# Kernel optimization log

Hardware: AMD Instinct MI355X
Metric: run time of the kernel (lower is better)

Reference implementation:

```python
import jax, jax.numpy as jnp
import numpy as np

N, E, B, D, H = 5000, 16000, 8, 128, 8
HD = D // H
DD = D // 2  # diachronic dim (gamma = 0.5)
V, R = 20000, 500


def setup_inputs() -> dict:
    key = jax.random.key(0)
    ks = jax.random.split(key, 28)
    f = lambda i, shape, s=0.05: (jax.random.normal(ks[i], shape, jnp.float32) * s)
    inp = {
        "src": jax.random.randint(ks[0], (E,), 0, N),
        "dst": jax.random.randint(ks[1], (E,), 0, N),
        "node_idx": jax.random.randint(ks[2], (N,), 0, V),
        "relation_type": jax.random.randint(ks[3], (E,), 1, R),
        "edge_start": jax.random.randint(ks[4], (E,), 0, 365),
        "edge_end": jax.random.randint(ks[5], (E,), 0, 365),
        "batch_start": jax.random.randint(ks[6], (B,), 0, 365),
        "batch_end": jax.random.randint(ks[7], (B,), 0, 365),
        "node_time": jax.random.uniform(ks[8], (N,), jnp.float32, 0.0, 365.0),
        "edge_t2v": f(9, (E, D), 1.0),
        "batch_t2v": f(10, (B, D), 1.0),
        "syn_embed": f(11, (V, D)),
        "dia_embed": f(12, (V, DD)),
        "dia_w": f(13, (V, DD)),
        "dia_b": f(14, (V, DD)),
        "rel_embed": f(15, (R, D)),
        "ts_W1": f(16, (2 * D, 4 * D)),
        "ts_b1": jnp.zeros((4 * D,), jnp.float32),
        "ts_W2": f(17, (4 * D, 2 * D)),
        "ts_b2": jnp.zeros((2 * D,), jnp.float32),
        "ts_W3": f(18, (2 * D, D)),
        "ts_b3": jnp.zeros((D,), jnp.float32),
        "W_ss": f(19, (3, D, D)),
        "b_ss": jnp.zeros((3, D), jnp.float32),
        "W_ee": f(20, (3, D, D)),
        "b_ee": jnp.zeros((3, D), jnp.float32),
        "attn_i": f(21, (H, HD), 0.1),
        "attn_j": f(22, (H, HD), 0.1),
    }
    return inp


def _lin3(x, idx, W, b):
    # x: (E,B,D); idx: (E,B) in {0:past,1:present,2:future}; W: (3,D,D); b: (3,D)
    out = jnp.zeros_like(x)
    for k in range(3):
        out = out + jnp.where((idx == k)[..., None], x @ W[k] + b[k], 0.0)
    return out


def reference(src, dst, node_idx, relation_type, edge_start, edge_end,
              batch_start, batch_end, node_time, edge_t2v, batch_t2v,
              syn_embed, dia_embed, dia_w, dia_b, rel_embed,
              ts_W1, ts_b1, ts_W2, ts_b2, ts_W3, ts_b3,
              W_ss, b_ss, W_ee, b_ee, attn_i, attn_j):
    # diachronic node embedding: synchronic + sin-modulated diachronic half
    h_n = syn_embed[node_idx]                                   # (N, D)
    dia = dia_embed[node_idx] * jnp.sin(
        dia_w[node_idx] * node_time[:, None] + dia_b[node_idx])  # (N, DD)
    h_n = h_n.at[:, DD:].add(dia)

    # tau: per-(edge, query) time score via MLP 2D -> 4D -> 2D -> D
    x = jnp.concatenate([
        jnp.broadcast_to(edge_t2v[:, None, :], (E, B, D)),
        jnp.broadcast_to(batch_t2v[None, :, :], (E, B, D))], axis=-1)
    h = jax.nn.relu(x @ ts_W1 + ts_b1)
    h = jax.nn.relu(h @ ts_W2 + ts_b2)
    tau = h @ ts_W3 + ts_b3                                      # (E, B, D)

    # time-type (past/present/future) selector per edge per query
    idx_ss = (jnp.sign(edge_start[:, None] - batch_start[None, :]) + 1).astype(jnp.int32)
    idx_ee = (jnp.sign(edge_end[:, None] - batch_end[None, :]) + 1).astype(jnp.int32)

    h_e = rel_embed[relation_type]                               # (E, D)
    g_e = (_lin3(h_n[src][:, None, :] + tau, idx_ss, W_ss, b_ss)
           + _lin3(h_e[:, None, :] + tau, idx_ee, W_ee, b_ee))   # (E, B, D)
    g_e = g_e.reshape(E, B, H, HD)

    # GAT-style scores: (dst-node * attn_i) * (edge * attn_j), elementwise per head
    ai = h_n.reshape(N, 1, H, HD) * attn_i                       # (N, 1, H, HD)
    score = jax.nn.leaky_relu(ai[dst] * (g_e * attn_j))          # (E, B, H, HD)

    # edge softmax per destination node (segment softmax over dst)
    m = jax.ops.segment_max(score, dst, num_segments=N)
    s = jnp.exp(score - m[dst])
    z = jax.ops.segment_sum(s, dst, num_segments=N)
    a = s / (z[dst] + 1e-16)

    h_new = jax.ops.segment_sum(a * g_e, dst, num_segments=N)    # (N, B, H, HD)
    return jax.nn.leaky_relu(h_new.reshape(N, B, D))
```

## Files before the change

kernel.cpp:

```cpp
#include <hip/hip_runtime.h>
#include <hip/hip_bf16.h>

typedef __attribute__((ext_vector_type(8))) short short8;
typedef __attribute__((ext_vector_type(4))) float f32x4;

#define N_NODES 5000
#define E_EDGES 16000
#define B_Q 8
#define D_DIM 128

#define OFF_U     0
#define OFF_G     4096000
#define OFF_HN    12288000
#define OFF_WDST  12928000
#define OFF_VB    13568000
#define OFF_W1T   13572096
#define OFF_W2T   13604864
#define OFF_W3T   13670400
#define OFF_WALLT 13686784
#define OFF_CNT   13735936
#define OFF_ROWP  13740936
#define OFF_CUR   13745937
#define OFF_ECSR  13750937
#define OFF_HSRC  13766944
#define OFF_HREL  14790944

__device__ __forceinline__ float leaky(float x) { return x > 0.f ? x : 0.01f * x; }
__device__ __forceinline__ int sgnk(int a, int b) { int d = a - b; return d > 0 ? 2 : (d == 0 ? 1 : 0); }
__device__ __forceinline__ unsigned short f2bf(float f) {
    __hip_bfloat16 h = __float2bfloat16(f);
    unsigned short r; __builtin_memcpy(&r, &h, 2); return r;
}
__device__ __forceinline__ unsigned pk2(float a, float b) {
    return (unsigned)f2bf(a) | ((unsigned)f2bf(b) << 16);
}
__device__ __forceinline__ float bflo(unsigned w) { return __uint_as_float(w << 16); }
__device__ __forceinline__ float bfhi(unsigned w) { return __uint_as_float(w & 0xffff0000u); }
__device__ __forceinline__ float bf2f(unsigned short s) { return __uint_as_float(((unsigned)s) << 16); }
__device__ __forceinline__ unsigned addpk(unsigned a, unsigned b) {
    return pk2(bflo(a) + bflo(b), bfhi(a) + bfhi(b));
}

#define SWZB(row, lb)  (((row) << 7) + ((lb) ^ (((row) & 7) << 4)))
#define SWZ256(row, lb) (((row) << 8) + ((lb) ^ (((row) & 7) << 4)))
#define SWZ512(row, lb) (((row) << 9) + ((lb) ^ (((row) & 7) << 4)))

__global__ void k_wprep(const float* __restrict__ W1, const float* __restrict__ W2,
                        const float* __restrict__ W3, const float* __restrict__ Wss,
                        const float* __restrict__ Wee,
                        ushort* __restrict__ W1t, ushort* __restrict__ W2t,
                        ushort* __restrict__ W3t, ushort* __restrict__ Wallt) {
    int tid = blockIdx.x * 256 + threadIdx.x;
    if (tid < 131072) {
        int n = tid >> 9, k = tid & 511;
        W2t[tid] = f2bf(W2[k * 256 + n]);
    } else if (tid < 163840) {
        int q = tid - 131072; int n = q >> 8, k = q & 255;
        W3t[q] = f2bf(W3[k * 128 + n]);
    } else if (tid < 262144) {
        int q = tid - 163840; int c = q >> 14, rr = q & 16383, n = rr >> 7, k = rr & 127;
        const float* Wm = (c < 3) ? Wss : Wee; int cc = (c < 3) ? c : c - 3;
        Wallt[q] = f2bf(Wm[cc * 16384 + k * 128 + n]);
    } else if (tid < 327680) {
        int q = tid - 262144; int n = q >> 7, k = q & 127;
        W1t[q] = f2bf(W1[k * 512 + n]);
    }
}

__global__ void k_node(const int* __restrict__ node_idx, const float* __restrict__ node_time,
                       const float* __restrict__ syn, const float* __restrict__ diae,
                       const float* __restrict__ diaw, const float* __restrict__ diab,
                       const float* __restrict__ attn_i, const float* __restrict__ attn_j,
                       float* __restrict__ h_n, float* __restrict__ w_dst) {
    int n = blockIdx.x, d = threadIdx.x;
    int nid = node_idx[n];
    float h = syn[nid * D_DIM + d];
    if (d >= 64) {
        int q = d - 64;
        h += diae[nid * 64 + q] * sinf(diaw[nid * 64 + q] * node_time[n] + diab[nid * 64 + q]);
    }
    h_n[n * D_DIM + d] = h;
    w_dst[n * D_DIM + d] = h * attn_i[d] * attn_j[d];
}

__global__ void k_vb(const float* __restrict__ bt2v, const float* __restrict__ W1,
                     const float* __restrict__ b1, float* __restrict__ v_b) {
    int b = blockIdx.x, j = threadIdx.x;
    float acc = b1[j];
    for (int i = 0; i < 128; ++i)
        acc = fmaf(bt2v[b * 128 + i], W1[(128 + i) * 512 + j], acc);
    v_b[b * 512 + j] = acc;
}

__global__ void k_egather(const int* __restrict__ src, const int* __restrict__ rtyp,
                          const float* __restrict__ h_n, const float* __restrict__ rel_embed,
                          ushort* __restrict__ hsrc, ushort* __restrict__ hrel) {
    int idx = blockIdx.x * 256 + threadIdx.x;
    int e = idx >> 7, d = idx & 127;
    hsrc[idx] = f2bf(h_n[src[e] * 128 + d]);
    hrel[idx] = f2bf(rel_embed[rtyp[e] * 128 + d]);
}

__global__ void k_count(const int* __restrict__ dst, int* __restrict__ cnt) {
    int e = blockIdx.x * 256 + threadIdx.x;
    if (e < E_EDGES) atomicAdd(&cnt[dst[e]], 1);
}

__global__ void k_scan(const int* __restrict__ cnt, int* __restrict__ rowptr,
                       int* __restrict__ cursor) {
    __shared__ int part[256];
    const int t = threadIdx.x;
    const int i0 = t * 20, i1 = min(N_NODES, i0 + 20);
    int s = 0;
    for (int i = i0; i < i1; ++i) s += cnt[i];
    part[t] = s;
    __syncthreads();
    for (int off = 1; off < 256; off <<= 1) {
        int v = (t >= off) ? part[t - off] : 0;
        __syncthreads();
        part[t] += v;
        __syncthreads();
    }
    int run = (t > 0) ? part[t - 1] : 0;
    for (int i = i0; i < i1; ++i) { rowptr[i] = run; cursor[i] = run; run += cnt[i]; }
    if (i0 < N_NODES && i1 == N_NODES) rowptr[N_NODES] = run;
}

__global__ void k_scatter(const int* __restrict__ dst, int* __restrict__ cursor,
                          int* __restrict__ ecsr) {
    int e = blockIdx.x * 256 + threadIdx.x;
    if (e < E_EDGES) {
        int p = atomicAdd(&cursor[dst[e]], 1);
        ecsr[p] = e;
    }
}

__device__ __forceinline__ void mfma_step(const unsigned char* lA, const unsigned char* lB,
                                          int wr, int wc, int lane, f32x4 (&acc)[4][4]) {
    const int row0 = wr * 64 + (lane & 15);
    const int nrow0 = wc * 64 + (lane & 15);
    const int kslot = (lane >> 4) * 16;
#pragma unroll
    for (int ks = 0; ks < 2; ++ks) {
        short8 a[4], b[4];
#pragma unroll
        for (int m = 0; m < 4; ++m)
            a[m] = *(const short8*)(lA + SWZB(row0 + m * 16, ks * 64 + kslot));
#pragma unroll
        for (int n = 0; n < 4; ++n)
            b[n] = *(const short8*)(lB + SWZB(nrow0 + n * 16, ks * 64 + kslot));
#pragma unroll
        for (int m = 0; m < 4; ++m)
#pragma unroll
            for (int n = 0; n < 4; ++n)
                acc[m][n] = __builtin_amdgcn_mfma_f32_16x16x32_bf16(a[m], b[n], acc[m][n], 0, 0, 0);
    }
}

__global__ __launch_bounds__(256) void k_gemm1(const float* __restrict__ et2v,
                                               const ushort* __restrict__ W1t,
                                               ushort* __restrict__ u) {
    __shared__ __align__(16) unsigned char lds2[32768];
    unsigned char* lA = lds2;
    unsigned char* lB = lds2 + 16384;
    const int t = threadIdx.x;
    const int m0 = (blockIdx.x >> 2) * 128;
    const int n0 = (blockIdx.x & 3) * 128;
    const int lane = t & 63, wid = t >> 6, wr = wid >> 1, wc = wid & 1;
    const int srow = t >> 1, koff = (t & 1) * 32, lb0 = (t & 1) * 64;
    f32x4 acc[4][4] = {};
    for (int step = 0; step < 2; ++step) {
        const float4* ap = (const float4*)(et2v + (size_t)(m0 + srow) * 128 + step * 64 + koff);
#pragma unroll
        for (int i = 0; i < 4; ++i) {
            float4 x0 = ap[2 * i], x1 = ap[2 * i + 1];
            *(uint4*)&lA[SWZB(srow, lb0 + i * 16)] =
                make_uint4(pk2(x0.x, x0.y), pk2(x0.z, x0.w), pk2(x1.x, x1.y), pk2(x1.z, x1.w));
        }
        const uint4* bp = (const uint4*)(W1t + (size_t)(n0 + srow) * 128 + step * 64 + koff);
#pragma unroll
        for (int i = 0; i < 4; ++i) *(uint4*)&lB[SWZB(srow, lb0 + i * 16)] = bp[i];
        __syncthreads();
        mfma_step(lA, lB, wr, wc, lane, acc);
        __syncthreads();
    }
    const int rbase = wr * 64 + ((lane >> 4) << 2);
    const int cb = wc * 64 + (lane & 15);
#pragma unroll
    for (int mm = 0; mm < 4; ++mm)
#pragma unroll
        for (int i = 0; i < 4; ++i) {
            const int r = rbase + mm * 16 + i;
#pragma unroll
            for (int nn = 0; nn < 4; ++nn)
                *(ushort*)&lds2[SWZ256(r, 2 * (cb + nn * 16))] = f2bf(acc[mm][nn][i]);
        }
    __syncthreads();
    {
        const int r = t >> 1, kh = t & 1;
        ushort* up = u + (size_t)(m0 + r) * 512 + n0 + kh * 64;
#pragma unroll
        for (int q = 0; q < 8; ++q)
            *(uint4*)(up + q * 8) = *(const uint4*)&lds2[SWZ256(r, kh * 128 + q * 16)];
    }
}

__global__ __launch_bounds__(256, 2) void k_mega(
    const ushort* __restrict__ u, const float* __restrict__ v_b,
    const ushort* __restrict__ W2t, const float* __restrict__ b2,
    const ushort* __restrict__ W3t, const float* __restrict__ b3,
    const ushort* __restrict__ Wallt,
    const float* __restrict__ bss, const float* __restrict__ bee,
    const ushort* __restrict__ hsrc, const ushort* __restrict__ hrel,
    const int* __restrict__ edge_start, const int* __restrict__ edge_end,
    const int* __restrict__ batch_start, const int* __restrict__ batch_end,
    ushort* __restrict__ g_e) {
    __shared__ __align__(16) unsigned char lds[65536];
    __shared__ __align__(16) float bsum[1152];
    __shared__ int selss_s[128], selee_s[128];
    __shared__ int am_s;
    const int t = threadIdx.x;
    const int m0 = blockIdx.x * 128;
    const int lane = t & 63, wid = t >> 6, wr = wid >> 1, wc = wid & 1;
    const int srow = t >> 1, koff = (t & 1) * 32, lb0 = (t & 1) * 64;
    const int l15 = lane & 15, ls4 = (lane >> 4) << 2;
    const int kslot = (lane >> 4) * 16, kslot8 = (lane >> 4) * 8;

    if (t == 0) am_s = 0;
    __syncthreads();
    if (t < 128) {
        const int gr = m0 + t, e = gr >> 3, b = gr & 7;
        const int ss = sgnk(edge_start[e], batch_start[b]);
        const int se = sgnk(edge_end[e], batch_end[b]);
        selss_s[t] = ss; selee_s[t] = se;
        atomicOr(&am_s, (1 << ss) | (8 << se));
    }
    for (int idx = t; idx < 1152; idx += 256) {
        const int combo = idx >> 7, k = idx & 127;
        bsum[idx] = bss[(combo / 3) * 128 + k] + bee[(combo % 3) * 128 + k];
    }

    unsigned char* lA = lds;
    unsigned char* lB = lds + 16384;
    const int ae = (m0 + srow) >> 3, ab = (m0 + srow) & 7;
    f32x4 acc2[4][8] = {};
    uint4 ucur[4], unxt[4];
    {
        const ushort* ub = u + (size_t)ae * 512 + koff;
#pragma unroll
        for (int i = 0; i < 4; ++i) ucur[i] = *(const uint4*)(ub + i * 8);
    }
    for (int step = 0; step < 8; ++step) {
        const int k0 = step * 64;
        const float4* vp = (const float4*)(v_b + ab * 512 + k0 + koff);
#pragma unroll
        for (int i = 0; i < 4; ++i) {
            uint4 uv = ucur[i];
            float4 va = vp[2 * i], vb4 = vp[2 * i + 1];
            unsigned r0 = pk2(fmaxf(bflo(uv.x) + va.x, 0.f), fmaxf(bfhi(uv.x) + va.y, 0.f));
            unsigned r1 = pk2(fmaxf(bflo(uv.y) + va.z, 0.f), fmaxf(bfhi(uv.y) + va.w, 0.f));
            unsigned r2 = pk2(fmaxf(bflo(uv.z) + vb4.x, 0.f), fmaxf(bfhi(uv.z) + vb4.y, 0.f));
            unsigned r3 = pk2(fmaxf(bflo(uv.w) + vb4.z, 0.f), fmaxf(bfhi(uv.w) + vb4.w, 0.f));
            *(uint4*)&lA[SWZB(srow, lb0 + i * 16)] = make_uint4(r0, r1, r2, r3);
        }
        const uint4* bp = (const uint4*)(W2t + (size_t)t * 512 + k0);
#pragma unroll
        for (int i = 0; i < 8; ++i) *(uint4*)&lB[SWZB(t, i * 16)] = bp[i];
        if (step < 7) {
            const ushort* ub = u + (size_t)ae * 512 + (k0 + 64) + koff;
#pragma unroll
            for (int i = 0; i < 4; ++i) unxt[i] = *(const uint4*)(ub + i * 8);
        }
        __syncthreads();
        {
            const int row0 = wr * 64 + l15;
            const int nrow0 = wc * 128 + l15;
#pragma unroll
            for (int ks = 0; ks < 2; ++ks) {
                short8 a[4], b[8];
#pragma unroll
                for (int m = 0; m < 4; ++m)
                    a[m] = *(const short8*)(lA + SWZB(row0 + m * 16, ks * 64 + kslot));
#pragma unroll
                for (int n = 0; n < 8; ++n)
                    b[n] = *(const short8*)(lB + SWZB(nrow0 + n * 16, ks * 64 + kslot));
#pragma unroll
                for (int m = 0; m < 4; ++m)
#pragma unroll
                    for (int n = 0; n < 8; ++n)
                        acc2[m][n] = __builtin_amdgcn_mfma_f32_16x16x32_bf16(a[m], b[n], acc2[m][n], 0, 0, 0);
            }
        }
        __syncthreads();
#pragma unroll
        for (int i = 0; i < 4; ++i) ucur[i] = unxt[i];
    }

    const int rb = wr * 64 + ls4;
    const int cb2 = wc * 128 + l15;
    float b2r[8];
#pragma unroll
    for (int nn = 0; nn < 8; ++nn) b2r[nn] = b2[cb2 + nn * 16];
#pragma unroll
    for (int mm = 0; mm < 4; ++mm)
#pragma unroll
        for (int i = 0; i < 4; ++i) {
            const int r = rb + mm * 16 + i;
#pragma unroll
            for (int nn = 0; nn < 8; ++nn) {
                const int k = cb2 + nn * 16;
                *(ushort*)&lds[SWZ512(r, 2 * k)] =
                    f2bf(fmaxf(acc2[mm][nn][i] + b2r[nn], 0.f));
            }
        }
    __syncthreads();

    f32x4 tacc[4][4] = {};
#pragma unroll
    for (int ks = 0; ks < 8; ++ks) {
        short8 a[4], b[4];
#pragma unroll
        for (int m = 0; m < 4; ++m) {
            const int rA = wr * 64 + l15 + m * 16;
            a[m] = *(const short8*)&lds[SWZ512(rA, ks * 64 + kslot)];
        }
#pragma unroll
        for (int n = 0; n < 4; ++n) {
            const int nB = wc * 64 + l15 + n * 16;
            b[n] = *(const short8*)(W3t + nB * 256 + ks * 32 + kslot8);
        }
#pragma unroll
        for (int m = 0; m < 4; ++m)
#pragma unroll
            for (int n = 0; n < 4; ++n)
                tacc[m][n] = __builtin_amdgcn_mfma_f32_16x16x32_bf16(a[m], b[n], tacc[m][n], 0, 0, 0);
    }
    __syncthreads();

    const int cb1 = wc * 64 + l15;
    float b3r[4];
#pragma unroll
    for (int nn = 0; nn < 4; ++nn) b3r[nn] = b3[cb1 + nn * 16];
#pragma unroll
    for (int mm = 0; mm < 4; ++mm)
#pragma unroll
        for (int i = 0; i < 4; ++i) {
            const int r = rb + mm * 16 + i;
#pragma unroll
            for (int nn = 0; nn < 4; ++nn) {
                const int k2 = cb1 + nn * 16;
                *(ushort*)&lds[SWZ256(r, 2 * k2)] = f2bf(tacc[mm][nn][i] + b3r[nn]);
            }
        }
    __syncthreads();

    {
        const int r = t >> 1, kh = t & 1, el = r >> 3;
        const ushort* hs = hsrc + ((size_t)(m0 >> 3) + el) * 128 + kh * 64;
        const ushort* hr = hrel + ((size_t)(m0 >> 3) + el) * 128 + kh * 64;
#pragma unroll
        for (int q = 0; q < 8; ++q) {
            const int boff = SWZ256(r, kh * 128 + q * 16);
            uint4 tv = *(const uint4*)&lds[boff];
            uint4 sv = *(const uint4*)(hs + q * 8);
            uint4 rv = *(const uint4*)(hr + q * 8);
            uint4 xs, xe;
            xs.x = addpk(tv.x, sv.x); xs.y = addpk(tv.y, sv.y);
            xs.z = addpk(tv.z, sv.z); xs.w = addpk(tv.w, sv.w);
            xe.x = addpk(tv.x, rv.x); xe.y = addpk(tv.y, rv.y);
            xe.z = addpk(tv.z, rv.z); xe.w = addpk(tv.w, rv.w);
            *(uint4*)&lds[boff] = xs;
            *(uint4*)&lds[32768 + boff] = xe;
        }
    }
    __syncthreads();

    int sel_ss[4], sel_ee[4];
#pragma unroll
    for (int m = 0; m < 4; ++m) {
        const int rA = wr * 64 + l15 + m * 16;
        sel_ss[m] = selss_s[rA]; sel_ee[m] = selee_s[rA];
    }
    const int am = am_s;
    const short8 zero8 = {0, 0, 0, 0, 0, 0, 0, 0};
    f32x4 gacc[4][4] = {};
    for (int c = 0; c < 6; ++c) {
        if (!((am >> c) & 1)) continue;
        const int m3 = (c < 3) ? c : c - 3;
        const int xb = (c < 3) ? 0 : 32768;
#pragma unroll
        for (int ks = 0; ks < 4; ++ks) {
            short8 a[4], b[4];
#pragma unroll
            for (int m = 0; m < 4; ++m) {
                const int rA = wr * 64 + l15 + m * 16;
                short8 v = *(const short8*)&lds[xb + SWZ256(rA, ks * 64 + kslot)];
                const int sel = (c < 3) ? sel_ss[m] : sel_ee[m];
                a[m] = (sel == m3) ? v : zero8;
            }
#pragma unroll
            for (int n = 0; n < 4; ++n) {
                const int nB = wc * 64 + l15 + n * 16;
                b[n] = *(const short8*)(Wallt + (size_t)c * 16384 + nB * 128 + ks * 32 + kslot8);
            }
#pragma unroll
            for (int m = 0; m < 4; ++m)
#pragma unroll
                for (int n = 0; n < 4; ++n)
                    gacc[m][n] = __builtin_amdgcn_mfma_f32_16x16x32_bf16(a[m], b[n], gacc[m][n], 0, 0, 0);
        }
    }
    __syncthreads();

#pragma unroll
    for (int mm = 0; mm < 4; ++mm)
#pragma unroll
        for (int i = 0; i < 4; ++i) {
            const int r = rb + mm * 16 + i;
#pragma unroll
            for (int nn = 0; nn < 4; ++nn) {
                const int k2 = cb1 + nn * 16;
                *(ushort*)&lds[SWZ256(r, 2 * k2)] = f2bf(gacc[mm][nn][i]);
            }
        }
    __syncthreads();
    {
        const int r = t >> 1, kh = t & 1;
        const int c9 = selss_s[r] * 3 + selee_s[r];
        const float* bp = &bsum[c9 * 128 + kh * 64];
        ushort* gp = g_e + (size_t)(m0 + r) * 128 + kh * 64;
#pragma unroll
        for (int q = 0; q < 8; ++q) {
            uint4 gv = *(const uint4*)&lds[SWZ256(r, kh * 128 + q * 16)];
            float4 f0 = *(const float4*)(bp + q * 8);
            float4 f1 = *(const float4*)(bp + q * 8 + 4);
            uint4 o;
            o.x = pk2(bflo(gv.x) + f0.x, bfhi(gv.x) + f0.y);
            o.y = pk2(bflo(gv.y) + f0.z, bfhi(gv.y) + f0.w);
            o.z = pk2(bflo(gv.z) + f1.x, bfhi(gv.z) + f1.y);
            o.w = pk2(bflo(gv.w) + f1.z, bfhi(gv.w) + f1.w);
            *(uint4*)(gp + q * 8) = o;
        }
    }
}

__global__ __launch_bounds__(128) void k_segsm(const int* __restrict__ rowptr,
                                               const int* __restrict__ ecsr,
                                               const float* __restrict__ wdst,
                                               const ushort* __restrict__ g_e,
                                               float* __restrict__ out) {
    const int n = blockIdx.x, d = threadIdx.x;
    const float w = wdst[n * 128 + d];
    const int s0 = rowptr[n], s1 = rowptr[n + 1];
    float m[8], z[8], S[8];
#pragma unroll
    for (int b = 0; b < 8; ++b) { m[b] = -1e30f; z[b] = 0.f; S[b] = 0.f; }
    for (int i = s0; i < s1; ++i) {
        const int e = ecsr[i];
        const ushort* gp = g_e + (size_t)e * 1024 + d;
#pragma unroll
        for (int b = 0; b < 8; ++b) {
            float g = bf2f(gp[b * 128]);
            float sc = leaky(w * g);
            float nm = fmaxf(m[b], sc);
            float sca = __expf(m[b] - nm);
            float s = __expf(sc - nm);
            z[b] = z[b] * sca + s;
            S[b] = S[b] * sca + s * g;
            m[b] = nm;
        }
    }
#pragma unroll
    for (int b = 0; b < 8; ++b) {
        float r = S[b] / (z[b] + 1e-16f);
        out[((size_t)n * 8 + b) * 128 + d] = leaky(r);
    }
}

extern "C" void kernel_launch(void* const* d_in, const int* in_sizes, int n_in,
                              void* d_out, int out_size, void* d_ws, size_t ws_size,
                              hipStream_t stream) {
    const int* src = (const int*)d_in[0];
    const int* dst = (const int*)d_in[1];
    const int* node_idx = (const int*)d_in[2];
    const int* rel = (const int*)d_in[3];
    const int* es = (const int*)d_in[4];
    const int* eend = (const int*)d_in[5];
    const int* bs = (const int*)d_in[6];
    const int* be = (const int*)d_in[7];
    const float* node_time = (const float*)d_in[8];
    const float* edge_t2v = (const float*)d_in[9];
    const float* batch_t2v = (const float*)d_in[10];
    const float* syn = (const float*)d_in[11];
    const float* diae = (const float*)d_in[12];
    const float* diaw = (const float*)d_in[13];
    const float* diab = (const float*)d_in[14];
    const float* rele = (const float*)d_in[15];
    const float* W1 = (const float*)d_in[16];
    const float* b1 = (const float*)d_in[17];
    const float* W2 = (const float*)d_in[18];
    const float* b2 = (const float*)d_in[19];
    const float* W3 = (const float*)d_in[20];
    const float* b3 = (const float*)d_in[21];
    const float* Wss = (const float*)d_in[22];
    const float* bss = (const float*)d_in[23];
    const float* Wee = (const float*)d_in[24];
    const float* bee = (const float*)d_in[25];
    const float* ai = (const float*)d_in[26];
    const float* aj = (const float*)d_in[27];

    float* ws = (float*)d_ws;
    ushort* u = (ushort*)(ws + OFF_U);
    ushort* g_e = (ushort*)(ws + OFF_G);
    float* h_n = ws + OFF_HN;
    float* wdst = ws + OFF_WDST;
    float* v_b = ws + OFF_VB;
    ushort* W1t = (ushort*)(ws + OFF_W1T);
    ushort* W2t = (ushort*)(ws + OFF_W2T);
    ushort* W3t = (ushort*)(ws + OFF_W3T);
    ushort* Wallt = (ushort*)(ws + OFF_WALLT);
    int* cnt = (int*)(ws + OFF_CNT);
    int* rowptr = (int*)(ws + OFF_ROWP);
    int* cursor = (int*)(ws + OFF_CUR);
    int* ecsr = (int*)(ws + OFF_ECSR);
    ushort* hsrc = (ushort*)(ws + OFF_HSRC);
    ushort* hrel = (ushort*)(ws + OFF_HREL);
    float* out = (float*)d_out;

    hipMemsetAsync(cnt, 0, N_NODES * sizeof(int), stream);
    k_count<<<63, 256, 0, stream>>>(dst, cnt);
    k_scan<<<1, 256, 0, stream>>>(cnt, rowptr, cursor);
    k_scatter<<<63, 256, 0, stream>>>(dst, cursor, ecsr);

    k_wprep<<<1280, 256, 0, stream>>>(W1, W2, W3, Wss, Wee, W1t, W2t, W3t, Wallt);
    k_node<<<N_NODES, 128, 0, stream>>>(node_idx, node_time, syn, diae, diaw, diab, ai, aj, h_n, wdst);
    k_vb<<<B_Q, 512, 0, stream>>>(batch_t2v, W1, b1, v_b);
    k_egather<<<E_EDGES * D_DIM / 256, 256, 0, stream>>>(src, rel, h_n, rele, hsrc, hrel);
    k_gemm1<<<500, 256, 0, stream>>>(edge_t2v, W1t, u);
    k_mega<<<1000, 256, 0, stream>>>(u, v_b, W2t, b2, W3t, b3, Wallt, bss, bee,
                                     hsrc, hrel, es, eend, bs, be, g_e);
    k_segsm<<<N_NODES, 128, 0, stream>>>(rowptr, ecsr, wdst, g_e, out);
}
```

Before: 340.3 us.

## Fuse edge-time GEMM into mega kernel and merge prep kernels

Removes the separate k_gemm1 launch and its u intermediate in global memory. Each k_mega block now computes its 16 edge rows of edge_t2v times W1 with MFMA and keeps the result in LDS, where it feeds the second MLP layer. The small prep kernels (weight transpose, node embedding, v_b, degree count, gather, scan) are merged into two multi-role launches to cut launch overhead. The trade-off is that the fused GEMM reads W1t directly from global memory without LDS staging. It also adds LDS pressure and serial work at the start of k_mega.

Result: faster. 325.0 us (-4.5%).

```diff
diff --git a/kernel.cpp b/kernel.cpp
--- a/kernel.cpp
+++ b/kernel.cpp
@@ -9,7 +9,6 @@
 #define B_Q 8
 #define D_DIM 128
 
-#define OFF_U     0
 #define OFF_G     4096000
 #define OFF_HN    12288000
 #define OFF_WDST  12928000
@@ -41,89 +40,97 @@
     return pk2(bflo(a) + bflo(b), bfhi(a) + bfhi(b));
 }
 
-#define SWZB(row, lb)  (((row) << 7) + ((lb) ^ (((row) & 7) << 4)))
-#define SWZ256(row, lb) (((row) << 8) + ((lb) ^ (((row) & 7) << 4)))
-#define SWZ512(row, lb) (((row) << 9) + ((lb) ^ (((row) & 7) << 4)))
-
-__global__ void k_wprep(const float* __restrict__ W1, const float* __restrict__ W2,
-                        const float* __restrict__ W3, const float* __restrict__ Wss,
-                        const float* __restrict__ Wee,
-                        ushort* __restrict__ W1t, ushort* __restrict__ W2t,
-                        ushort* __restrict__ W3t, ushort* __restrict__ Wallt) {
-    int tid = blockIdx.x * 256 + threadIdx.x;
-    if (tid < 131072) {
-        int n = tid >> 9, k = tid & 511;
-        W2t[tid] = f2bf(W2[k * 256 + n]);
-    } else if (tid < 163840) {
-        int q = tid - 131072; int n = q >> 8, k = q & 255;
-        W3t[q] = f2bf(W3[k * 128 + n]);
-    } else if (tid < 262144) {
-        int q = tid - 163840; int c = q >> 14, rr = q & 16383, n = rr >> 7, k = rr & 127;
-        const float* Wm = (c < 3) ? Wss : Wee; int cc = (c < 3) ? c : c - 3;
-        Wallt[q] = f2bf(Wm[cc * 16384 + k * 128 + n]);
-    } else if (tid < 327680) {
-        int q = tid - 262144; int n = q >> 7, k = q & 127;
-        W1t[q] = f2bf(W1[k * 512 + n]);
-    }
-}
-
-__global__ void k_node(const int* __restrict__ node_idx, const float* __restrict__ node_time,
-                       const float* __restrict__ syn, const float* __restrict__ diae,
-                       const float* __restrict__ diaw, const float* __restrict__ diab,
-                       const float* __restrict__ attn_i, const float* __restrict__ attn_j,
-                       float* __restrict__ h_n, float* __restrict__ w_dst) {
-    int n = blockIdx.x, d = threadIdx.x;
-    int nid = node_idx[n];
-    float h = syn[nid * D_DIM + d];
-    if (d >= 64) {
-        int q = d - 64;
-        h += diae[nid * 64 + q] * sinf(diaw[nid * 64 + q] * node_time[n] + diab[nid * 64 + q]);
-    }
-    h_n[n * D_DIM + d] = h;
-    w_dst[n * D_DIM + d] = h * attn_i[d] * attn_j[d];
-}
-
-__global__ void k_vb(const float* __restrict__ bt2v, const float* __restrict__ W1,
-                     const float* __restrict__ b1, float* __restrict__ v_b) {
-    int b = blockIdx.x, j = threadIdx.x;
-    float acc = b1[j];
-    for (int i = 0; i < 128; ++i)
-        acc = fmaf(bt2v[b * 128 + i], W1[(128 + i) * 512 + j], acc);
-    v_b[b * 512 + j] = acc;
-}
-
-__global__ void k_egather(const int* __restrict__ src, const int* __restrict__ rtyp,
-                          const float* __restrict__ h_n, const float* __restrict__ rel_embed,
-                          ushort* __restrict__ hsrc, ushort* __restrict__ hrel) {
-    int idx = blockIdx.x * 256 + threadIdx.x;
-    int e = idx >> 7, d = idx & 127;
-    hsrc[idx] = f2bf(h_n[src[e] * 128 + d]);
-    hrel[idx] = f2bf(rel_embed[rtyp[e] * 128 + d]);
-}
-
-__global__ void k_count(const int* __restrict__ dst, int* __restrict__ cnt) {
-    int e = blockIdx.x * 256 + threadIdx.x;
-    if (e < E_EDGES) atomicAdd(&cnt[dst[e]], 1);
-}
-
-__global__ void k_scan(const int* __restrict__ cnt, int* __restrict__ rowptr,
-                       int* __restrict__ cursor) {
-    __shared__ int part[256];
-    const int t = threadIdx.x;
-    const int i0 = t * 20, i1 = min(N_NODES, i0 + 20);
-    int s = 0;
-    for (int i = i0; i < i1; ++i) s += cnt[i];
-    part[t] = s;
-    __syncthreads();
-    for (int off = 1; off < 256; off <<= 1) {
-        int v = (t >= off) ? part[t - off] : 0;
+#define SWZB(row, lb)   (((row) << 7)  + ((lb) ^ (((row) & 7) << 4)))
+#define SWZ256(row, lb) (((row) << 8)  + ((lb) ^ (((row) & 7) << 4)))
+#define SWZ512(row, lb) (((row) << 9)  + ((lb) ^ (((row) & 7) << 4)))
+#define SWZ1K(row, lb)  (((row) << 10) + ((lb) ^ (((row) & 7) << 4)))
+
+__global__ __launch_bounds__(256) void k_prepA(
+    const float* __restrict__ W1, const float* __restrict__ W2,
+    const float* __restrict__ W3, const float* __restrict__ Wss,
+    const float* __restrict__ Wee,
+    const int* __restrict__ node_idx, const float* __restrict__ node_time,
+    const float* __restrict__ syn, const float* __restrict__ diae,
+    const float* __restrict__ diaw, const float* __restrict__ diab,
+    const float* __restrict__ attn_i, const float* __restrict__ attn_j,
+    const float* __restrict__ bt2v, const float* __restrict__ b1,
+    const int* __restrict__ dst,
+    ushort* __restrict__ W1t, ushort* __restrict__ W2t,
+    ushort* __restrict__ W3t, ushort* __restrict__ Wallt,
+    float* __restrict__ h_n, float* __restrict__ w_dst,
+    float* __restrict__ v_b, int* __restrict__ cnt) {
+    const int bid = blockIdx.x, t = threadIdx.x;
+    if (bid < 1280) {
+        int tid = bid * 256 + t;
+        if (tid < 131072) {
+            int n = tid >> 9, k = tid & 511;
+            W2t[tid] = f2bf(W2[k * 256 + n]);
+        } else if (tid < 163840) {
+            int q = tid - 131072; int n = q >> 8, k = q & 255;
+            W3t[q] = f2bf(W3[k * 128 + n]);
+        } else if (tid < 262144) {
+            int q = tid - 163840; int c = q >> 14, rr = q & 16383, n = rr >> 7, k = rr & 127;
+            const float* Wm = (c < 3) ? Wss : Wee; int cc = (c < 3) ? c : c - 3;
+            Wallt[q] = f2bf(Wm[cc * 16384 + k * 128 + n]);
+        } else if (tid < 327680) {
+            int q = tid - 262144; int n = q >> 7, k = q & 127;
+            W1t[q] = f2bf(W1[k * 512 + n]);
+        }
+    } else if (bid < 3780) {
+        int n = (bid - 1280) * 2 + (t >> 7), d = t & 127;
+        int nid = node_idx[n];
+        float h = syn[nid * D_DIM + d];
+        if (d >= 64) {
+            int q = d - 64;
+            h += diae[nid * 64 + q] * sinf(diaw[nid * 64 + q] * node_time[n] + diab[nid * 64 + q]);
+        }
+        h_n[n * D_DIM + d] = h;
+        w_dst[n * D_DIM + d] = h * attn_i[d] * attn_j[d];
+    } else if (bid < 3788) {
+        int b = bid - 3780;
+#pragma unroll
+        for (int jj = 0; jj < 2; ++jj) {
+            int j = t + jj * 256;
+            float acc = b1[j];
+            for (int i = 0; i < 128; ++i)
+                acc = fmaf(bt2v[b * 128 + i], W1[(128 + i) * 512 + j], acc);
+            v_b[b * 512 + j] = acc;
+        }
+    } else {
+        int e = (bid - 3788) * 256 + t;
+        if (e < E_EDGES) atomicAdd(&cnt[dst[e]], 1);
+    }
+}
+
+__global__ __launch_bounds__(256) void k_prepB(
+    const int* __restrict__ src, const int* __restrict__ rtyp,
+    const float* __restrict__ h_n, const float* __restrict__ rel_embed,
+    const int* __restrict__ cnt,
+    ushort* __restrict__ hsrc, ushort* __restrict__ hrel,
+    int* __restrict__ rowptr, int* __restrict__ cursor) {
+    const int bid = blockIdx.x, t = threadIdx.x;
+    if (bid < 8000) {
+        int idx = bid * 256 + t;
+        int e = idx >> 7, d = idx & 127;
+        hsrc[idx] = f2bf(h_n[src[e] * 128 + d]);
+        hrel[idx] = f2bf(rel_embed[rtyp[e] * 128 + d]);
+    } else {
+        __shared__ int part[256];
+        const int i0 = t * 20, i1 = min(N_NODES, i0 + 20);
+        int s = 0;
+        for (int i = i0; i < i1; ++i) s += cnt[i];
+        part[t] = s;
         __syncthreads();
-        part[t] += v;
-        __syncthreads();
-    }
-    int run = (t > 0) ? part[t - 1] : 0;
-    for (int i = i0; i < i1; ++i) { rowptr[i] = run; cursor[i] = run; run += cnt[i]; }
-    if (i0 < N_NODES && i1 == N_NODES) rowptr[N_NODES] = run;
+        for (int off = 1; off < 256; off <<= 1) {
+            int v = (t >= off) ? part[t - off] : 0;
+            __syncthreads();
+            part[t] += v;
+            __syncthreads();
+        }
+        int run = (t > 0) ? part[t - 1] : 0;
+        for (int i = i0; i < i1; ++i) { rowptr[i] = run; cursor[i] = run; run += cnt[i]; }
+        if (i0 < N_NODES && i1 == N_NODES) rowptr[N_NODES] = run;
+    }
 }
 
 __global__ void k_scatter(const int* __restrict__ dst, int* __restrict__ cursor,
@@ -135,78 +142,9 @@
     }
 }
 
-__device__ __forceinline__ void mfma_step(const unsigned char* lA, const unsigned char* lB,
-                                          int wr, int wc, int lane, f32x4 (&acc)[4][4]) {
-    const int row0 = wr * 64 + (lane & 15);
-    const int nrow0 = wc * 64 + (lane & 15);
-    const int kslot = (lane >> 4) * 16;
-#pragma unroll
-    for (int ks = 0; ks < 2; ++ks) {
-        short8 a[4], b[4];
-#pragma unroll
-        for (int m = 0; m < 4; ++m)
-            a[m] = *(const short8*)(lA + SWZB(row0 + m * 16, ks * 64 + kslot));
-#pragma unroll
-        for (int n = 0; n < 4; ++n)
-            b[n] = *(const short8*)(lB + SWZB(nrow0 + n * 16, ks * 64 + kslot));
-#pragma unroll
-        for (int m = 0; m < 4; ++m)
-#pragma unroll
-            for (int n = 0; n < 4; ++n)
-                acc[m][n] = __builtin_amdgcn_mfma_f32_16x16x32_bf16(a[m], b[n], acc[m][n], 0, 0, 0);
-    }
-}
-
-__global__ __launch_bounds__(256) void k_gemm1(const float* __restrict__ et2v,
-                                               const ushort* __restrict__ W1t,
-                                               ushort* __restrict__ u) {
-    __shared__ __align__(16) unsigned char lds2[32768];
-    unsigned char* lA = lds2;
-    unsigned char* lB = lds2 + 16384;
-    const int t = threadIdx.x;
-    const int m0 = (blockIdx.x >> 2) * 128;
-    const int n0 = (blockIdx.x & 3) * 128;
-    const int lane = t & 63, wid = t >> 6, wr = wid >> 1, wc = wid & 1;
-    const int srow = t >> 1, koff = (t & 1) * 32, lb0 = (t & 1) * 64;
-    f32x4 acc[4][4] = {};
-    for (int step = 0; step < 2; ++step) {
-        const float4* ap = (const float4*)(et2v + (size_t)(m0 + srow) * 128 + step * 64 + koff);
-#pragma unroll
-        for (int i = 0; i < 4; ++i) {
-            float4 x0 = ap[2 * i], x1 = ap[2 * i + 1];
-            *(uint4*)&lA[SWZB(srow, lb0 + i * 16)] =
-                make_uint4(pk2(x0.x, x0.y), pk2(x0.z, x0.w), pk2(x1.x, x1.y), pk2(x1.z, x1.w));
-        }
-        const uint4* bp = (const uint4*)(W1t + (size_t)(n0 + srow) * 128 + step * 64 + koff);
-#pragma unroll
-        for (int i = 0; i < 4; ++i) *(uint4*)&lB[SWZB(srow, lb0 + i * 16)] = bp[i];
-        __syncthreads();
-        mfma_step(lA, lB, wr, wc, lane, acc);
-        __syncthreads();
-    }
-    const int rbase = wr * 64 + ((lane >> 4) << 2);
-    const int cb = wc * 64 + (lane & 15);
-#pragma unroll
-    for (int mm = 0; mm < 4; ++mm)
-#pragma unroll
-        for (int i = 0; i < 4; ++i) {
-            const int r = rbase + mm * 16 + i;
-#pragma unroll
-            for (int nn = 0; nn < 4; ++nn)
-                *(ushort*)&lds2[SWZ256(r, 2 * (cb + nn * 16))] = f2bf(acc[mm][nn][i]);
-        }
-    __syncthreads();
-    {
-        const int r = t >> 1, kh = t & 1;
-        ushort* up = u + (size_t)(m0 + r) * 512 + n0 + kh * 64;
-#pragma unroll
-        for (int q = 0; q < 8; ++q)
-            *(uint4*)(up + q * 8) = *(const uint4*)&lds2[SWZ256(r, kh * 128 + q * 16)];
-    }
-}
-
 __global__ __launch_bounds__(256, 2) void k_mega(
-    const ushort* __restrict__ u, const float* __restrict__ v_b,
+    const float* __restrict__ et2v, const ushort* __restrict__ W1t,
+    const float* __restrict__ v_b,
     const ushort* __restrict__ W2t, const float* __restrict__ b2,
     const ushort* __restrict__ W3t, const float* __restrict__ b3,
     const ushort* __restrict__ Wallt,
@@ -221,6 +159,7 @@
     __shared__ int am_s;
     const int t = threadIdx.x;
     const int m0 = blockIdx.x * 128;
+    const int e0 = m0 >> 3;
     const int lane = t & 63, wid = t >> 6, wr = wid >> 1, wc = wid & 1;
     const int srow = t >> 1, koff = (t & 1) * 32, lb0 = (t & 1) * 64;
     const int l15 = lane & 15, ls4 = (lane >> 4) << 2;
@@ -240,22 +179,48 @@
         bsum[idx] = bss[(combo / 3) * 128 + k] + bee[(combo % 3) * 128 + k];
     }
 
+    {
+        const int row = t >> 4, col8 = (t & 15) * 8;
+        const float4* ep = (const float4*)(et2v + ((size_t)(e0 + row)) * 128 + col8);
+        float4 x0 = ep[0], x1 = ep[1];
+        *(uint4*)&lds[SWZ256(row, 2 * col8)] =
+            make_uint4(pk2(x0.x, x0.y), pk2(x0.z, x0.w), pk2(x1.x, x1.y), pk2(x1.z, x1.w));
+    }
+    __syncthreads();
+    {
+        f32x4 acc1[8] = {};
+#pragma unroll
+        for (int ks = 0; ks < 4; ++ks) {
+            short8 a = *(const short8*)&lds[SWZ256(l15, ks * 64 + kslot)];
+#pragma unroll
+            for (int n = 0; n < 8; ++n) {
+                const int nB = wid * 128 + n * 16 + l15;
+                short8 b = *(const short8*)(W1t + (size_t)nB * 128 + ks * 32 + kslot8);
+                acc1[n] = __builtin_amdgcn_mfma_f32_16x16x32_bf16(a, b, acc1[n], 0, 0, 0);
+            }
+        }
+        __syncthreads();
+#pragma unroll
+        for (int n = 0; n < 8; ++n)
+#pragma unroll
+            for (int i = 0; i < 4; ++i) {
+                const int r = (lane >> 4) * 4 + i;
+                const int cc = wid * 128 + n * 16 + l15;
+                *(ushort*)&lds[49152 + SWZ1K(r, 2 * cc)] = f2bf(acc1[n][i]);
+            }
+    }
+    __syncthreads();
+
     unsigned char* lA = lds;
     unsigned char* lB = lds + 16384;
-    const int ae = (m0 + srow) >> 3, ab = (m0 + srow) & 7;
+    const int urow = srow >> 3, ab = (m0 + srow) & 7;
     f32x4 acc2[4][8] = {};
-    uint4 ucur[4], unxt[4];
-    {
-        const ushort* ub = u + (size_t)ae * 512 + koff;
-#pragma unroll
-        for (int i = 0; i < 4; ++i) ucur[i] = *(const uint4*)(ub + i * 8);
-    }
     for (int step = 0; step < 8; ++step) {
         const int k0 = step * 64;
         const float4* vp = (const float4*)(v_b + ab * 512 + k0 + koff);
 #pragma unroll
         for (int i = 0; i < 4; ++i) {
-            uint4 uv = ucur[i];
+            uint4 uv = *(const uint4*)&lds[49152 + SWZ1K(urow, 2 * (k0 + koff) + i * 16)];
             float4 va = vp[2 * i], vb4 = vp[2 * i + 1];
             unsigned r0 = pk2(fmaxf(bflo(uv.x) + va.x, 0.f), fmaxf(bfhi(uv.x) + va.y, 0.f));
             unsigned r1 = pk2(fmaxf(bflo(uv.y) + va.z, 0.f), fmaxf(bfhi(uv.y) + va.w, 0.f));
@@ -266,11 +231,6 @@
         const uint4* bp = (const uint4*)(W2t + (size_t)t * 512 + k0);
 #pragma unroll
         for (int i = 0; i < 8; ++i) *(uint4*)&lB[SWZB(t, i * 16)] = bp[i];
-        if (step < 7) {
-            const ushort* ub = u + (size_t)ae * 512 + (k0 + 64) + koff;
-#pragma unroll
-            for (int i = 0; i < 4; ++i) unxt[i] = *(const uint4*)(ub + i * 8);
-        }
         __syncthreads();
         {
             const int row0 = wr * 64 + l15;
@@ -292,8 +252,6 @@
             }
         }
         __syncthreads();
-#pragma unroll
-        for (int i = 0; i < 4; ++i) ucur[i] = unxt[i];
     }
 
     const int rb = wr * 64 + ls4;
@@ -356,8 +314,8 @@
 
     {
         const int r = t >> 1, kh = t & 1, el = r >> 3;
-        const ushort* hs = hsrc + ((size_t)(m0 >> 3) + el) * 128 + kh * 64;
-        const ushort* hr = hrel + ((size_t)(m0 >> 3) + el) * 128 + kh * 64;
+        const ushort* hs = hsrc + ((size_t)e0 + el) * 128 + kh * 64;
+        const ushort* hr = hrel + ((size_t)e0 + el) * 128 + kh * 64;
 #pragma unroll
         for (int q = 0; q < 8; ++q) {
             const int boff = SWZ256(r, kh * 128 + q * 16);
@@ -510,7 +468,6 @@
     const float* aj = (const float*)d_in[27];
 
     float* ws = (float*)d_ws;
-    ushort* u = (ushort*)(ws + OFF_U);
     ushort* g_e = (ushort*)(ws + OFF_G);
     float* h_n = ws + OFF_HN;
     float* wdst = ws + OFF_WDST;
@@ -528,16 +485,13 @@
     float* out = (float*)d_out;
 
     hipMemsetAsync(cnt, 0, N_NODES * sizeof(int), stream);
-    k_count<<<63, 256, 0, stream>>>(dst, cnt);
-    k_scan<<<1, 256, 0, stream>>>(cnt, rowptr, cursor);
+    k_prepA<<<3851, 256, 0, stream>>>(W1, W2, W3, Wss, Wee,
+                                      node_idx, node_time, syn, diae, diaw, diab, ai, aj,
+                                      batch_t2v, b1, dst,
+                                      W1t, W2t, W3t, Wallt, h_n, wdst, v_b, cnt);
+    k_prepB<<<8001, 256, 0, stream>>>(src, rel, h_n, rele, cnt, hsrc, hrel, rowptr, cursor);
     k_scatter<<<63, 256, 0, stream>>>(dst, cursor, ecsr);
-
-    k_wprep<<<1280, 256, 0, stream>>>(W1, W2, W3, Wss, Wee, W1t, W2t, W3t, Wallt);
-    k_node<<<N_NODES, 128, 0, stream>>>(node_idx, node_time, syn, diae, diaw, diab, ai, aj, h_n, wdst);
-    k_vb<<<B_Q, 512, 0, stream>>>(batch_t2v, W1, b1, v_b);
-    k_egather<<<E_EDGES * D_DIM / 256, 256, 0, stream>>>(src, rel, h_n, rele, hsrc, hrel);
-    k_gemm1<<<500, 256, 0, stream>>>(edge_t2v, W1t, u);
-    k_mega<<<1000, 256, 0, stream>>>(u, v_b, W2t, b2, W3t, b3, Wallt, bss, bee,
+    k_mega<<<1000, 256, 0, stream>>>(edge_t2v, W1t, v_b, W2t, b2, W3t, b3, Wallt, bss, bee,
                                      hsrc, hrel, es, eend, bs, be, g_e);
     k_segsm<<<N_NODES, 128, 0, stream>>>(rowptr, ecsr, wdst, g_e, out);
 }
```
